# Performance work log

Measured on AMD Instinct MI355X. Metric: run time of the kernel, lower is better.

Reference implementation:

```python
import jax, jax.numpy as jnp
import numpy as np

B, T, C = 4, 1024, 768
H, HS = 12, 64           # num_heads, head_size
VD = 2 * HS              # value dim per head


def setup_inputs() -> dict:
    key = jax.random.key(0)
    ks = jax.random.split(key, 16)
    s = 0.02
    inp = {
        "x": jax.random.normal(ks[0], (B, T, C), jnp.float32),
        "Wq1": jax.random.normal(ks[1], (H, C, HS), jnp.float32) * s,
        "Wk1": jax.random.normal(ks[2], (H, C, HS), jnp.float32) * s,
        "Wq2": jax.random.normal(ks[3], (H, C, HS), jnp.float32) * s,
        "Wk2": jax.random.normal(ks[4], (H, C, HS), jnp.float32) * s,
        "Wv": jax.random.normal(ks[5], (H, C, VD), jnp.float32) * s,
        "lq1": jax.random.normal(ks[6], (H, HS), jnp.float32) * 0.1,
        "lk1": jax.random.normal(ks[7], (H, HS), jnp.float32) * 0.1,
        "lq2": jax.random.normal(ks[8], (H, HS), jnp.float32) * 0.1,
        "lk2": jax.random.normal(ks[9], (H, HS), jnp.float32) * 0.1,
        "gn_w": jnp.ones((H * VD,), jnp.float32),
        "gn_b": jnp.zeros((H * VD,), jnp.float32),
        "Wp": jax.random.normal(ks[10], (C, H * VD), jnp.float32) * s,
        "bp": jnp.zeros((C,), jnp.float32),
        "layer_idx": 3,
    }
    return inp


def _diff_attn(x, Wq1, Wk1, Wq2, Wk2, Wv, lq1, lk1, lq2, lk2,
               gn_w, gn_b, Wp, bp, layer_idx):
    Bc, Tc, _ = x.shape
    scale = 1.0 / jnp.sqrt(jnp.float32(HS))
    # per-head projections: [B,H,T,HS]
    q1 = jnp.einsum('btc,hcd->bhtd', x, Wq1)
    k1 = jnp.einsum('btc,hcd->bhtd', x, Wk1)
    q2 = jnp.einsum('btc,hcd->bhtd', x, Wq2)
    k2 = jnp.einsum('btc,hcd->bhtd', x, Wk2)
    v = jnp.einsum('btc,hce->bhte', x, Wv)           # [B,H,T,2HS]
    mask = jnp.tril(jnp.ones((Tc, Tc), bool))         # causal
    neg = jnp.float32(-jnp.inf)
    a1 = jnp.einsum('bhtd,bhsd->bhts', q1, k1) * scale
    a2 = jnp.einsum('bhtd,bhsd->bhts', q2, k2) * scale
    a1 = jax.nn.softmax(jnp.where(mask, a1, neg), axis=-1)
    a2 = jax.nn.softmax(jnp.where(mask, a2, neg), axis=-1)
    # dynamic lambda init, per get_lambda
    li = jnp.float32(layer_idx)
    dyn = 0.8 - 0.6 * jnp.exp(-0.3 * (li - 1.0))
    lam = jnp.mean(jnp.exp(lq1 * lk1) - jnp.exp(lq2 * lk2) + dyn, axis=-1)  # [H]
    diff = a1 - lam[None, :, None, None] * a2
    out = jnp.einsum('bhts,bhse->bhte', diff, v)      # [B,H,T,2HS]
    out = out.transpose(0, 2, 1, 3).reshape(Bc, Tc, H * VD)
    # GroupLayerNorm == full layernorm over last dim (unbiased=False var)
    mu = out.mean(-1, keepdims=True)
    var = jnp.mean((out - mu) ** 2, axis=-1, keepdims=True)
    out = (out - mu) / jnp.sqrt(var + 1e-5) * gn_w + gn_b
    out = out * 0.2  # (1 - lambda_init_buffer=0.8), buffer never updated
    return out @ Wp.T + bp


def reference(x, Wq1, Wk1, Wq2, Wk2, Wv, lq1, lk1, lq2, lk2,
              gn_w, gn_b, Wp, bp, layer_idx):
    return _diff_attn(x, Wq1, Wk1, Wq2, Wk2, Wv, lq1, lk1, lq2, lk2,
                      gn_w, gn_b, Wp, bp, layer_idx)
```

## Files before the change

### kernel.cpp

```cpp
#include <hip/hip_runtime.h>
#include <hip/hip_bf16.h>

#define Bc   4
#define Tc   1024
#define Cc   768
#define Hc   12
#define HSc  64
#define VDc  128
#define NQKV 4608
#define YLD  3072
#define NROWS 4096
#define HVD  1536

#define Q1OFF 0
#define K1OFF 768
#define Q2OFF 1536
#define K2OFF 2304

typedef __bf16 bf16x8 __attribute__((ext_vector_type(8)));
typedef float f32x4 __attribute__((ext_vector_type(4)));

#define PW_S 36
#define EXP2SCALE 0.18033688011112042f

static __device__ __forceinline__ float bf2f(unsigned short s) {
    return __uint_as_float(((unsigned int)s) << 16);
}
static __device__ __forceinline__ unsigned short f2bf(float f) {
    unsigned int u = __float_as_uint(f);
    unsigned int r = (u + 0x7FFFu + ((u >> 16) & 1u)) >> 16;
    return (unsigned short)r;
}
static __device__ __forceinline__ unsigned int pack2bf(float lo, float hi) {
    unsigned int a = (__float_as_uint(lo) + 0x8000u) >> 16;
    unsigned int b = (__float_as_uint(hi) + 0x8000u) & 0xFFFF0000u;
    return a | b;
}

static __device__ __forceinline__ void load16_lds(const void* g, void* l) {
    __builtin_amdgcn_global_load_lds(
        (const __attribute__((address_space(1))) void*)g,
        (__attribute__((address_space(3))) void*)l, 16, 0, 0);
}

__global__ __launch_bounds__(256) void cast_bf16(
    const float* __restrict__ src, unsigned short* __restrict__ dst)
{
    int i = blockIdx.x * 256 + threadIdx.x;
    float4 v = *(const float4*)(src + (size_t)i * 4);
    ushort4 u;
    u.x = f2bf(v.x); u.y = f2bf(v.y); u.z = f2bf(v.z); u.w = f2bf(v.w);
    *(ushort4*)(dst + (size_t)i * 4) = u;
}

__global__ __launch_bounds__(256) void trans_w(
    const float* __restrict__ Wq1, const float* __restrict__ Wk1,
    const float* __restrict__ Wq2, const float* __restrict__ Wk2,
    const float* __restrict__ Wv, unsigned short* __restrict__ WcatT)
{
    __shared__ float tile[64][65];
    int tid = threadIdx.x;
    int t = blockIdx.x;
    int kt = t % 12, nt = t / 12;
    int k0 = kt * 64, n0 = nt * 64;
    const float* src;
    int stride;
    if (n0 < 3072) {
        int which = n0 / 768, m = n0 - which * 768, h = m >> 6;
        const float* W = (which == 0) ? Wq1 : (which == 1) ? Wk1 : (which == 2) ? Wq2 : Wk2;
        src = W + ((size_t)h * 768 + k0) * 64;
        stride = 64;
    } else {
        int rel = n0 - 3072, h = rel >> 7, e0 = rel & 127;
        src = Wv + ((size_t)h * 768 + k0) * 128 + e0;
        stride = 128;
    }
    for (int i = tid; i < 4096; i += 256) {
        int kl = i >> 6, dl = i & 63;
        tile[dl][kl] = src[(size_t)kl * stride + dl];
    }
    __syncthreads();
    for (int i = tid; i < 4096; i += 256) {
        int nl = i >> 6, kl = i & 63;
        WcatT[(size_t)(n0 + nl) * 768 + k0 + kl] = f2bf(tile[nl][kl]);
    }
}

__global__ __launch_bounds__(64) void lambda_kernel(
    const float* __restrict__ lq1, const float* __restrict__ lk1,
    const float* __restrict__ lq2, const float* __restrict__ lk2,
    const int* __restrict__ layer_idx, float* __restrict__ lam)
{
    int h = blockIdx.x, l = threadIdx.x;
    float li = (float)layer_idx[0];
    float dyn = 0.8f - 0.6f * expf(-0.3f * (li - 1.0f));
    int i = h * HSc + l;
    float v = expf(lq1[i] * lk1[i]) - expf(lq2[i] * lk2[i]) + dyn;
    #pragma unroll
    for (int off = 32; off; off >>= 1) v += __shfl_xor(v, off);
    if (l == 0) lam[h] = v * (1.0f / 64.0f);
}

template<int TN, int KD, int LDC, bool OUT_BIAS, bool SPLITV>
__global__ __launch_bounds__(256) void gemm_mfma(
    const unsigned short* __restrict__ A, const unsigned short* __restrict__ Bt,
    unsigned short* __restrict__ Cb, float* __restrict__ Cf,
    const float* __restrict__ bias, unsigned short* __restrict__ VtOut)
{
    constexpr int BN = TN * 32;
    constexpr int JB = TN / 2;
    __shared__ unsigned short As[128 * 32];
    __shared__ unsigned short Bs[BN * 32];
    int tid = threadIdx.x, lane = tid & 63, w = tid >> 6;
    int wm = w >> 1, wn = w & 1;
    int m0 = blockIdx.y * 128, n0 = blockIdx.x * BN;

    int lr = lane >> 2, lq = lane & 3;
    const unsigned short* gA[2];
    const unsigned short* gB[JB];
    #pragma unroll
    for (int j = 0; j < 2; ++j) {
        int row = w * 32 + j * 16 + lr;
        int qg = lq ^ ((row >> 1) & 3);
        gA[j] = A + (size_t)(m0 + row) * KD + qg * 8;
    }
    #pragma unroll
    for (int j = 0; j < JB; ++j) {
        int row = w * (JB * 16) + j * 16 + lr;
        int qg = lq ^ ((row >> 1) & 3);
        gB[j] = Bt + (size_t)(n0 + row) * KD + qg * 8;
    }

    int rr = lane & 15, qd = lane >> 4;
    const unsigned short* aAddr[4];
    const unsigned short* bAddr[TN];
    #pragma unroll
    for (int i = 0; i < 4; ++i) {
        int row = wm * 64 + i * 16 + rr;
        int qs = qd ^ ((row >> 1) & 3);
        aAddr[i] = As + row * 32 + qs * 8;
    }
    #pragma unroll
    for (int t = 0; t < TN; ++t) {
        int row = wn * (TN * 16) + t * 16 + rr;
        int qs = qd ^ ((row >> 1) & 3);
        bAddr[t] = Bs + row * 32 + qs * 8;
    }

    f32x4 acc[4][TN];
    #pragma unroll
    for (int i = 0; i < 4; ++i)
        #pragma unroll
        for (int t = 0; t < TN; ++t) acc[i][t] = {0.f, 0.f, 0.f, 0.f};

    for (int k = 0; k < KD / 32; ++k) {
        __syncthreads();
        load16_lds(gA[0], As + (w * 2 + 0) * 512);
        load16_lds(gA[1], As + (w * 2 + 1) * 512);
        #pragma unroll
        for (int j = 0; j < JB; ++j)
            load16_lds(gB[j], Bs + (w * JB + j) * 512);
        gA[0] += 32; gA[1] += 32;
        #pragma unroll
        for (int j = 0; j < JB; ++j) gB[j] += 32;
        __syncthreads();

        bf16x8 af[4], bfr[TN];
        #pragma unroll
        for (int i = 0; i < 4; ++i) af[i] = *(const bf16x8*)aAddr[i];
        #pragma unroll
        for (int t = 0; t < TN; ++t) bfr[t] = *(const bf16x8*)bAddr[t];
        #pragma unroll
        for (int i = 0; i < 4; ++i)
            #pragma unroll
            for (int t = 0; t < TN; ++t)
                acc[i][t] = __builtin_amdgcn_mfma_f32_16x16x32_bf16(af[i], bfr[t], acc[i][t], 0, 0, 0);
    }

    #pragma unroll
    for (int t = 0; t < TN; ++t) {
        int col = n0 + wn * (TN * 16) + t * 16 + rr;
        if (SPLITV && col >= 3072) {
            int rel = col - 3072, hh = rel >> 7, e = rel & 127;
            #pragma unroll
            for (int i = 0; i < 4; ++i) {
                int row0 = m0 + wm * 64 + i * 16 + qd * 4;
                int b = row0 >> 10, tt = row0 & 1023;
                ushort4 pk;
                pk.x = f2bf(acc[i][t][0]); pk.y = f2bf(acc[i][t][1]);
                pk.z = f2bf(acc[i][t][2]); pk.w = f2bf(acc[i][t][3]);
                *(ushort4*)&VtOut[(size_t)((b * Hc + hh) * 128 + e) * 1024 + tt] = pk;
            }
        } else {
            float bv = OUT_BIAS ? bias[col] : 0.f;
            #pragma unroll
            for (int i = 0; i < 4; ++i) {
                #pragma unroll
                for (int r = 0; r < 4; ++r) {
                    int row = m0 + wm * 64 + i * 16 + qd * 4 + r;
                    if (OUT_BIAS)
                        Cf[(size_t)row * LDC + col] = acc[i][t][r] + bv;
                    else
                        Cb[(size_t)row * LDC + col] = f2bf(acc[i][t][r]);
                }
            }
        }
    }
}

__global__ __launch_bounds__(128, 2) void diff_attn_mfma(
    const unsigned short* __restrict__ Y, const unsigned short* __restrict__ Vt,
    const float* __restrict__ lam_buf, unsigned short* __restrict__ attn)
{
    __shared__ unsigned int PL32[2][16 * PW_S];
    int bh = blockIdx.x;
    int b = bh / Hc, h = bh - b * Hc;
    int QT = 31 - (int)blockIdx.y;
    int tid = threadIdx.x, lane = tid & 63, wv = tid >> 6;
    int cl = lane & 15, qd = lane >> 4;
    float lamv = lam_buf[h];
    size_t rowbase = (size_t)(b * Tc) * YLD;
    const int hq = h * HSc;
    unsigned int* Pw = PL32[wv];
    const unsigned short* VtB = Vt + ((size_t)bh << 17);
    const f32x4 zero4 = {0.f, 0.f, 0.f, 0.f};

    bf16x8 ka[2][4], kb[2][4], va[8], vb2[8];

    auto loadK = [&](int kt, bf16x8 kf[2][4]) {
        #pragma unroll
        for (int c = 0; c < 2; ++c) {
            size_t koff = rowbase + (size_t)(kt * 32 + c * 16 + cl) * YLD;
            kf[c][0] = *(const bf16x8*)(Y + koff + K1OFF + hq + qd * 8);
            kf[c][1] = *(const bf16x8*)(Y + koff + K1OFF + hq + 32 + qd * 8);
            kf[c][2] = *(const bf16x8*)(Y + koff + K2OFF + hq + qd * 8);
            kf[c][3] = *(const bf16x8*)(Y + koff + K2OFF + hq + 32 + qd * 8);
        }
    };
    auto loadV = [&](int kt, bf16x8 vf[8]) {
        #pragma unroll
        for (int ec = 0; ec < 8; ++ec)
            vf[ec] = *(const bf16x8*)(VtB + (((ec * 16 + cl) << 10) + kt * 32 + qd * 8));
    };

    int qrow = QT * 32 + wv * 16;

    size_t qoff = rowbase + (size_t)(qrow + cl) * YLD;
    bf16x8 q1a = *(const bf16x8*)(Y + qoff + Q1OFF + hq + qd * 8);
    bf16x8 q1b = *(const bf16x8*)(Y + qoff + Q1OFF + hq + 32 + qd * 8);
    bf16x8 q2a = *(const bf16x8*)(Y + qoff + Q2OFF + hq + qd * 8);
    bf16x8 q2b = *(const bf16x8*)(Y + qoff + Q2OFF + hq + 32 + qd * 8);

    f32x4 O1[8], O2[8];
    #pragma unroll
    for (int ec = 0; ec < 8; ++ec) { O1[ec] = zero4; O2[ec] = zero4; }
    float l1[4] = {0.f, 0.f, 0.f, 0.f}, l2[4] = {0.f, 0.f, 0.f, 0.f};

    auto tile = [&](int kt, bf16x8 kf[2][4], bf16x8 vf[8], bool diag) {
        f32x4 S1[2], S2[2];
        #pragma unroll
        for (int c = 0; c < 2; ++c) { S1[c] = zero4; S2[c] = zero4; }
        #pragma unroll
        for (int c = 0; c < 2; ++c) {
            S1[c] = __builtin_amdgcn_mfma_f32_16x16x32_bf16(q1a, kf[c][0], S1[c], 0, 0, 0);
            S1[c] = __builtin_amdgcn_mfma_f32_16x16x32_bf16(q1b, kf[c][1], S1[c], 0, 0, 0);
            S2[c] = __builtin_amdgcn_mfma_f32_16x16x32_bf16(q2a, kf[c][2], S2[c], 0, 0, 0);
            S2[c] = __builtin_amdgcn_mfma_f32_16x16x32_bf16(q2b, kf[c][3], S2[c], 0, 0, 0);
        }
        if (diag) {
            #pragma unroll
            for (int c = 0; c < 2; ++c) {
                int key_local = c * 16 + cl;
                #pragma unroll
                for (int r = 0; r < 4; ++r) {
                    int row_local = wv * 16 + qd * 4 + r;
                    if (key_local > row_local) { S1[c][r] = -1e30f; S2[c][r] = -1e30f; }
                }
            }
        }
        #pragma unroll
        for (int r = 0; r < 4; ++r) {
            float p10 = exp2f(S1[0][r] * EXP2SCALE);
            float p11 = exp2f(S1[1][r] * EXP2SCALE);
            float p20 = exp2f(S2[0][r] * EXP2SCALE);
            float p21 = exp2f(S2[1][r] * EXP2SCALE);
            l1[r] += p10 + p11;
            l2[r] += p20 + p21;
            int row = (qd << 2) + r;
            Pw[row * PW_S + cl]      = pack2bf(p10, p20);
            Pw[row * PW_S + cl + 16] = pack2bf(p11, p21);
        }
        const unsigned int* rp = Pw + cl * PW_S + qd * 8;
        uint4 L0 = *(const uint4*)(rp);
        uint4 L1 = *(const uint4*)(rp + 4);
        uint4 u1, u2;
        u1.x = __builtin_amdgcn_perm(L0.y, L0.x, 0x05040100u);
        u1.y = __builtin_amdgcn_perm(L0.w, L0.z, 0x05040100u);
        u1.z = __builtin_amdgcn_perm(L1.y, L1.x, 0x05040100u);
        u1.w = __builtin_amdgcn_perm(L1.w, L1.z, 0x05040100u);
        u2.x = __builtin_amdgcn_perm(L0.y, L0.x, 0x07060302u);
        u2.y = __builtin_amdgcn_perm(L0.w, L0.z, 0x07060302u);
        u2.z = __builtin_amdgcn_perm(L1.y, L1.x, 0x07060302u);
        u2.w = __builtin_amdgcn_perm(L1.w, L1.z, 0x07060302u);
        bf16x8 pa1 = __builtin_bit_cast(bf16x8, u1);
        bf16x8 pa2 = __builtin_bit_cast(bf16x8, u2);
        #pragma unroll
        for (int ec = 0; ec < 8; ++ec) {
            O1[ec] = __builtin_amdgcn_mfma_f32_16x16x32_bf16(pa1, vf[ec], O1[ec], 0, 0, 0);
            O2[ec] = __builtin_amdgcn_mfma_f32_16x16x32_bf16(pa2, vf[ec], O2[ec], 0, 0, 0);
        }
    };

    loadK(0, ka); loadV(0, va);
    for (int kt = 0; kt <= QT; kt += 2) {
        if (kt + 1 <= QT) { loadK(kt + 1, kb); loadV(kt + 1, vb2); }
        tile(kt, ka, va, kt == QT);
        if (kt + 1 <= QT) {
            if (kt + 2 <= QT) { loadK(kt + 2, ka); loadV(kt + 2, va); }
            tile(kt + 1, kb, vb2, kt + 1 == QT);
        }
    }

    float w1[4], w2[4];
    #pragma unroll
    for (int r = 0; r < 4; ++r) {
        float a = l1[r], c = l2[r];
        a += __shfl_xor(a, 1); a += __shfl_xor(a, 2);
        a += __shfl_xor(a, 4); a += __shfl_xor(a, 8);
        c += __shfl_xor(c, 1); c += __shfl_xor(c, 2);
        c += __shfl_xor(c, 4); c += __shfl_xor(c, 8);
        w1[r] = 1.0f / a;
        w2[r] = lamv / c;
    }
    #pragma unroll
    for (int ec = 0; ec < 8; ++ec) {
        #pragma unroll
        for (int r = 0; r < 4; ++r) {
            size_t row = (size_t)(b * Tc + qrow + qd * 4 + r);
            attn[row * HVD + h * VDc + ec * 16 + cl] =
                f2bf(O1[ec][r] * w1[r] - O2[ec][r] * w2[r]);
        }
    }
}

__global__ __launch_bounds__(128) void ln_inplace(
    unsigned short* __restrict__ attn,
    const float* __restrict__ gnw, const float* __restrict__ gnb)
{
    int row = blockIdx.x, tid = threadIdx.x;
    unsigned short* p = attn + (size_t)row * HVD;
    float v[12];
    float s = 0.f, sq = 0.f;
    #pragma unroll
    for (int j = 0; j < 3; ++j) {
        int g = tid + j * 128;
        ushort4 u = *(const ushort4*)(p + g * 4);
        float x0 = bf2f(u.x), x1 = bf2f(u.y), x2 = bf2f(u.z), x3 = bf2f(u.w);
        v[j * 4 + 0] = x0; v[j * 4 + 1] = x1; v[j * 4 + 2] = x2; v[j * 4 + 3] = x3;
        s += x0 + x1 + x2 + x3;
        sq = fmaf(x0, x0, sq); sq = fmaf(x1, x1, sq);
        sq = fmaf(x2, x2, sq); sq = fmaf(x3, x3, sq);
    }
    #pragma unroll
    for (int off = 32; off; off >>= 1) { s += __shfl_xor(s, off); sq += __shfl_xor(sq, off); }
    __shared__ float ss[2], sqs[2];
    if ((tid & 63) == 0) { ss[tid >> 6] = s; sqs[tid >> 6] = sq; }
    __syncthreads();
    float S = ss[0] + ss[1], Q = sqs[0] + sqs[1];
    float mu = S * (1.0f / HVD);
    float rstd = rsqrtf(Q * (1.0f / HVD) - mu * mu + 1e-5f);
    #pragma unroll
    for (int j = 0; j < 3; ++j) {
        int g = tid + j * 128;
        float4 gw = *(const float4*)(gnw + g * 4);
        float4 gb = *(const float4*)(gnb + g * 4);
        ushort4 o;
        o.x = f2bf(((v[j * 4 + 0] - mu) * rstd * gw.x + gb.x) * 0.2f);
        o.y = f2bf(((v[j * 4 + 1] - mu) * rstd * gw.y + gb.y) * 0.2f);
        o.z = f2bf(((v[j * 4 + 2] - mu) * rstd * gw.z + gb.z) * 0.2f);
        o.w = f2bf(((v[j * 4 + 3] - mu) * rstd * gw.w + gb.w) * 0.2f);
        *(ushort4*)(p + g * 4) = o;
    }
}

extern "C" void kernel_launch(void* const* d_in, const int* in_sizes, int n_in,
                              void* d_out, int out_size, void* d_ws, size_t ws_size,
                              hipStream_t stream)
{
    const float* x   = (const float*)d_in[0];
    const float* Wq1 = (const float*)d_in[1];
    const float* Wk1 = (const float*)d_in[2];
    const float* Wq2 = (const float*)d_in[3];
    const float* Wk2 = (const float*)d_in[4];
    const float* Wv  = (const float*)d_in[5];
    const float* lq1 = (const float*)d_in[6];
    const float* lk1 = (const float*)d_in[7];
    const float* lq2 = (const float*)d_in[8];
    const float* lk2 = (const float*)d_in[9];
    const float* gnw = (const float*)d_in[10];
    const float* gnb = (const float*)d_in[11];
    const float* Wp  = (const float*)d_in[12];
    const float* bp  = (const float*)d_in[13];
    const int*   lidx = (const int*)d_in[14];
    float* out = (float*)d_out;

    char* w = (char*)d_ws;
    unsigned short* WcatT = (unsigned short*)(w);
    unsigned short* Xb    = (unsigned short*)(w + 7077888);
    unsigned short* Y     = (unsigned short*)(w + 13369344);
    unsigned short* VtW   = (unsigned short*)(w + 38535168);
    unsigned short* attn  = (unsigned short*)(w + 51118080);
    unsigned short* Wpb   = (unsigned short*)(w + 63700992);
    float* lam            = (float*)(w + 66060288);

    cast_bf16<<<dim3(NROWS * Cc / 1024), 256, 0, stream>>>(x, Xb);
    cast_bf16<<<dim3(Cc * HVD / 1024), 256, 0, stream>>>(Wp, Wpb);
    trans_w<<<dim3(72 * 12), 256, 0, stream>>>(Wq1, Wk1, Wq2, Wk2, Wv, WcatT);
    lambda_kernel<<<dim3(Hc), 64, 0, stream>>>(lq1, lk1, lq2, lk2, lidx, lam);
    gemm_mfma<4, 768, YLD, false, true><<<dim3(NQKV / 128, NROWS / 128), 256, 0, stream>>>(
        Xb, WcatT, Y, nullptr, nullptr, VtW);
    diff_attn_mfma<<<dim3(Bc * Hc, 32), 128, 0, stream>>>(Y, VtW, lam, attn);
    ln_inplace<<<dim3(NROWS), 128, 0, stream>>>(attn, gnw, gnb);
    gemm_mfma<2, HVD, Cc, true, false><<<dim3(Cc / 64, NROWS / 128), 256, 0, stream>>>(
        attn, Wpb, nullptr, out, bp, nullptr);
}
```

Before: 292.3 us.

## Split attention key range across two wave pairs and reduce via LDS

The attention kernel now launches 256 threads per block: each pair of waves processes half of the key tiles for the same 32 query rows, a split-K over the causal key range. Partial O1/O2 accumulators and row sums from the second half are exchanged through shared memory and added by the first half, which then normalizes and writes the output. This doubles the waves available per block to hide latency and shortens the per-wave serial loop for long rows, at the cost of extra LDS traffic, three block barriers and higher shared memory use per block. No max-subtraction is used, so the partial sums combine without any rescaling.

```diff
diff --git a/kernel.cpp b/kernel.cpp
--- a/kernel.cpp
+++ b/kernel.cpp
@@ -208,15 +208,20 @@
     }
 }
 
-__global__ __launch_bounds__(128, 2) void diff_attn_mfma(
+__global__ __launch_bounds__(256, 4) void diff_attn_mfma(
     const unsigned short* __restrict__ Y, const unsigned short* __restrict__ Vt,
     const float* __restrict__ lam_buf, unsigned short* __restrict__ attn)
 {
-    __shared__ unsigned int PL32[2][16 * PW_S];
+    __shared__ __align__(16) unsigned int PL32[4][16 * PW_S];
+    __shared__ __align__(16) float Oex[2][128][20];
+    __shared__ float lex[2][16][2];
+
     int bh = blockIdx.x;
     int b = bh / Hc, h = bh - b * Hc;
     int QT = 31 - (int)blockIdx.y;
     int tid = threadIdx.x, lane = tid & 63, wv = tid >> 6;
+    int rg = wv & 1;
+    int sh = wv >> 1;
     int cl = lane & 15, qd = lane >> 4;
     float lamv = lam_buf[h];
     size_t rowbase = (size_t)(b * Tc) * YLD;
@@ -243,7 +248,7 @@
             vf[ec] = *(const bf16x8*)(VtB + (((ec * 16 + cl) << 10) + kt * 32 + qd * 8));
     };
 
-    int qrow = QT * 32 + wv * 16;
+    int qrow = QT * 32 + rg * 16;
 
     size_t qoff = rowbase + (size_t)(qrow + cl) * YLD;
     bf16x8 q1a = *(const bf16x8*)(Y + qoff + Q1OFF + hq + qd * 8);
@@ -273,7 +278,7 @@
                 int key_local = c * 16 + cl;
                 #pragma unroll
                 for (int r = 0; r < 4; ++r) {
-                    int row_local = wv * 16 + qd * 4 + r;
+                    int row_local = rg * 16 + qd * 4 + r;
                     if (key_local > row_local) { S1[c][r] = -1e30f; S2[c][r] = -1e30f; }
                 }
             }
@@ -311,17 +316,22 @@
         }
     };
 
-    loadK(0, ka); loadV(0, va);
-    for (int kt = 0; kt <= QT; kt += 2) {
-        if (kt + 1 <= QT) { loadK(kt + 1, kb); loadV(kt + 1, vb2); }
+    int n = QT + 1;
+    int nh = (n + 1) >> 1;
+    int lo = sh ? nh : 0;
+    int hi = sh ? n : nh;
+
+    if (lo < hi) { loadK(lo, ka); loadV(lo, va); }
+    for (int kt = lo; kt < hi; kt += 2) {
+        if (kt + 1 < hi) { loadK(kt + 1, kb); loadV(kt + 1, vb2); }
         tile(kt, ka, va, kt == QT);
-        if (kt + 1 <= QT) {
-            if (kt + 2 <= QT) { loadK(kt + 2, ka); loadV(kt + 2, va); }
+        if (kt + 1 < hi) {
+            if (kt + 2 < hi) { loadK(kt + 2, ka); loadV(kt + 2, va); }
             tile(kt + 1, kb, vb2, kt + 1 == QT);
         }
     }
 
-    float w1[4], w2[4];
+    float la1[4], la2[4];
     #pragma unroll
     for (int r = 0; r < 4; ++r) {
         float a = l1[r], c = l2[r];
@@ -329,16 +339,58 @@
         a += __shfl_xor(a, 4); a += __shfl_xor(a, 8);
         c += __shfl_xor(c, 1); c += __shfl_xor(c, 2);
         c += __shfl_xor(c, 4); c += __shfl_xor(c, 8);
-        w1[r] = 1.0f / a;
-        w2[r] = lamv / c;
-    }
-    #pragma unroll
-    for (int ec = 0; ec < 8; ++ec) {
+        la1[r] = a; la2[r] = c;
+    }
+
+    if (sh == 1) {
+        #pragma unroll
+        for (int ec = 0; ec < 8; ++ec)
+            *(f32x4*)&Oex[rg][ec * 16 + cl][qd * 4] = O1[ec];
+        if (cl == 0) {
+            #pragma unroll
+            for (int r = 0; r < 4; ++r) {
+                lex[rg][qd * 4 + r][0] = la1[r];
+                lex[rg][qd * 4 + r][1] = la2[r];
+            }
+        }
+    }
+    __syncthreads();
+    if (sh == 0) {
+        #pragma unroll
+        for (int ec = 0; ec < 8; ++ec)
+            O1[ec] += *(const f32x4*)&Oex[rg][ec * 16 + cl][qd * 4];
         #pragma unroll
         for (int r = 0; r < 4; ++r) {
-            size_t row = (size_t)(b * Tc + qrow + qd * 4 + r);
-            attn[row * HVD + h * VDc + ec * 16 + cl] =
-                f2bf(O1[ec][r] * w1[r] - O2[ec][r] * w2[r]);
+            la1[r] += lex[rg][qd * 4 + r][0];
+            la2[r] += lex[rg][qd * 4 + r][1];
+        }
+    }
+    __syncthreads();
+    if (sh == 1) {
+        #pragma unroll
+        for (int ec = 0; ec < 8; ++ec)
+            *(f32x4*)&Oex[rg][ec * 16 + cl][qd * 4] = O2[ec];
+    }
+    __syncthreads();
+    if (sh == 0) {
+        #pragma unroll
+        for (int ec = 0; ec < 8; ++ec)
+            O2[ec] += *(const f32x4*)&Oex[rg][ec * 16 + cl][qd * 4];
+
+        float w1[4], w2[4];
+        #pragma unroll
+        for (int r = 0; r < 4; ++r) {
+            w1[r] = 1.0f / la1[r];
+            w2[r] = lamv / la2[r];
+        }
+        #pragma unroll
+        for (int ec = 0; ec < 8; ++ec) {
+            #pragma unroll
+            for (int r = 0; r < 4; ++r) {
+                size_t row = (size_t)(b * Tc + qrow + qd * 4 + r);
+                attn[row * HVD + h * VDc + ec * 16 + cl] =
+                    f2bf(O1[ec][r] * w1[r] - O2[ec][r] * w2[r]);
+            }
         }
     }
 }
@@ -419,7 +471,7 @@
     lambda_kernel<<<dim3(Hc), 64, 0, stream>>>(lq1, lk1, lq2, lk2, lidx, lam);
     gemm_mfma<4, 768, YLD, false, true><<<dim3(NQKV / 128, NROWS / 128), 256, 0, stream>>>(
         Xb, WcatT, Y, nullptr, nullptr, VtW);
-    diff_attn_mfma<<<dim3(Bc * Hc, 32), 128, 0, stream>>>(Y, VtW, lam, attn);
+    diff_attn_mfma<<<dim3(Bc * Hc, 32), 256, 0, stream>>>(Y, VtW, lam, attn);
     ln_inplace<<<dim3(NROWS), 128, 0, stream>>>(attn, gnw, gnb);
     gemm_mfma<2, HVD, Cc, true, false><<<dim3(Cc / 64, NROWS / 128), 256, 0, stream>>>(
         attn, Wpb, nullptr, out, bp, nullptr);
```

Result: slower. 482.6 us (+65.1%).

## Stage K/V tiles through swizzled shared memory shared by four-wave query blocks

Applied to the files above, without the earlier changes.

The attention kernel now processes 64 query rows per block with four waves. K and V tiles are staged cooperatively into double-buffered, XOR-swizzled LDS via direct global-to-LDS loads, and all waves read their fragments from there. Before, each wave loaded its own K/V fragments from global memory into registers. The aim is to cut redundant global K/V traffic and raise reuse, at the cost of a block-wide barrier per key tile and idle waves on the diagonal tail.

```diff
diff --git a/kernel.cpp b/kernel.cpp
--- a/kernel.cpp
+++ b/kernel.cpp
@@ -208,14 +208,16 @@
     }
 }
 
-__global__ __launch_bounds__(128, 2) void diff_attn_mfma(
+__global__ __launch_bounds__(256) void diff_attn_mfma(
     const unsigned short* __restrict__ Y, const unsigned short* __restrict__ Vt,
     const float* __restrict__ lam_buf, unsigned short* __restrict__ attn)
 {
-    __shared__ unsigned int PL32[2][16 * PW_S];
+    __shared__ __align__(16) unsigned short KV[2][8192];
+    __shared__ __align__(16) unsigned int PL32[4][16 * PW_S];
+
     int bh = blockIdx.x;
     int b = bh / Hc, h = bh - b * Hc;
-    int QT = 31 - (int)blockIdx.y;
+    int g = 15 - (int)blockIdx.y;
     int tid = threadIdx.x, lane = tid & 63, wv = tid >> 6;
     int cl = lane & 15, qd = lane >> 4;
     float lamv = lam_buf[h];
@@ -225,25 +227,57 @@
     const unsigned short* VtB = Vt + ((size_t)bh << 17);
     const f32x4 zero4 = {0.f, 0.f, 0.f, 0.f};
 
-    bf16x8 ka[2][4], kb[2][4], va[8], vb2[8];
-
-    auto loadK = [&](int kt, bf16x8 kf[2][4]) {
-        #pragma unroll
-        for (int c = 0; c < 2; ++c) {
-            size_t koff = rowbase + (size_t)(kt * 32 + c * 16 + cl) * YLD;
-            kf[c][0] = *(const bf16x8*)(Y + koff + K1OFF + hq + qd * 8);
-            kf[c][1] = *(const bf16x8*)(Y + koff + K1OFF + hq + 32 + qd * 8);
-            kf[c][2] = *(const bf16x8*)(Y + koff + K2OFF + hq + qd * 8);
-            kf[c][3] = *(const bf16x8*)(Y + koff + K2OFF + hq + 32 + qd * 8);
+    int ksrow = lane >> 3;
+    int ksch  = (lane & 7) ^ ksrow;
+    int offk[4];
+    {
+        int mat = wv & 1;
+        int moff = mat ? K2OFF : K1OFF;
+        #pragma unroll
+        for (int r8 = 0; r8 < 4; ++r8)
+            offk[r8] = (r8 * 8 + ksrow) * YLD + moff + hq + ksch * 8;
+    }
+    int vsel = lane >> 2;
+    int vsch = (lane & 3) ^ (vsel & 3);
+    int offv[4];
+    {
+        int sv0 = (wv & 1) * 4;
+        #pragma unroll
+        for (int i = 0; i < 4; ++i)
+            offv[i] = ((sv0 + i) * 16 + vsel) * 1024 + vsch * 8;
+    }
+
+    auto stage = [&](int kt, int cur) {
+        char* base = (char*)KV[cur] + wv * 4096;
+        if (wv < 2) {
+            const unsigned short* g0 = Y + rowbase + (size_t)(kt * 32) * YLD;
+            #pragma unroll
+            for (int r8 = 0; r8 < 4; ++r8)
+                load16_lds(g0 + offk[r8], base + r8 * 1024);
+        } else {
+            const unsigned short* g0 = VtB + kt * 32;
+            #pragma unroll
+            for (int i = 0; i < 4; ++i)
+                load16_lds(g0 + offv[i], base + i * 1024);
         }
     };
-    auto loadV = [&](int kt, bf16x8 vf[8]) {
-        #pragma unroll
-        for (int ec = 0; ec < 8; ++ec)
-            vf[ec] = *(const bf16x8*)(VtB + (((ec * 16 + cl) << 10) + kt * 32 + qd * 8));
-    };
-
-    int qrow = QT * 32 + wv * 16;
+
+    int kfo[2][4], vfo[8];
+    #pragma unroll
+    for (int c = 0; c < 2; ++c) {
+        int row = c * 16 + cl;
+        #pragma unroll
+        for (int j = 0; j < 4; ++j)
+            kfo[c][j] = (j >> 1) * 4096 + row * 128 +
+                        ((((j & 1) * 4 + qd) ^ (row & 7)) << 4);
+    }
+    #pragma unroll
+    for (int ec = 0; ec < 8; ++ec) {
+        int e = ec * 16 + cl;
+        vfo[ec] = 8192 + e * 64 + ((qd ^ (e & 3)) << 4);
+    }
+
+    int qrow = g * 64 + wv * 16;
 
     size_t qoff = rowbase + (size_t)(qrow + cl) * YLD;
     bf16x8 q1a = *(const bf16x8*)(Y + qoff + Q1OFF + hq + qd * 8);
@@ -256,7 +290,15 @@
     for (int ec = 0; ec < 8; ++ec) { O1[ec] = zero4; O2[ec] = zero4; }
     float l1[4] = {0.f, 0.f, 0.f, 0.f}, l2[4] = {0.f, 0.f, 0.f, 0.f};
 
-    auto tile = [&](int kt, bf16x8 kf[2][4], bf16x8 vf[8], bool diag) {
+    auto tile = [&](int cur, int kt, bool diag) {
+        const char* kb = (const char*)KV[cur];
+        bf16x8 kf[2][4];
+        #pragma unroll
+        for (int c = 0; c < 2; ++c)
+            #pragma unroll
+            for (int j = 0; j < 4; ++j)
+                kf[c][j] = *(const bf16x8*)(kb + kfo[c][j]);
+
         f32x4 S1[2], S2[2];
         #pragma unroll
         for (int c = 0; c < 2; ++c) { S1[c] = zero4; S2[c] = zero4; }
@@ -270,14 +312,18 @@
         if (diag) {
             #pragma unroll
             for (int c = 0; c < 2; ++c) {
-                int key_local = c * 16 + cl;
+                int kq = kt * 32 + c * 16 + cl - qrow - qd * 4;
                 #pragma unroll
                 for (int r = 0; r < 4; ++r) {
-                    int row_local = wv * 16 + qd * 4 + r;
-                    if (key_local > row_local) { S1[c][r] = -1e30f; S2[c][r] = -1e30f; }
+                    if (kq > r) { S1[c][r] = -1e30f; S2[c][r] = -1e30f; }
                 }
             }
         }
+        bf16x8 vf[8];
+        #pragma unroll
+        for (int ec = 0; ec < 8; ++ec)
+            vf[ec] = *(const bf16x8*)(kb + vfo[ec]);
+
         #pragma unroll
         for (int r = 0; r < 4; ++r) {
             float p10 = exp2f(S1[0][r] * EXP2SCALE);
@@ -311,14 +357,19 @@
         }
     };
 
-    loadK(0, ka); loadV(0, va);
-    for (int kt = 0; kt <= QT; kt += 2) {
-        if (kt + 1 <= QT) { loadK(kt + 1, kb); loadV(kt + 1, vb2); }
-        tile(kt, ka, va, kt == QT);
-        if (kt + 1 <= QT) {
-            if (kt + 2 <= QT) { loadK(kt + 2, ka); loadV(kt + 2, va); }
-            tile(kt + 1, kb, vb2, kt + 1 == QT);
-        }
+    int NT = 2 * g + 2;
+    int ktmax = 2 * g + (wv >> 1);
+
+    stage(0, 0);
+    __syncthreads();
+    for (int kt = 0; kt < NT; ++kt) {
+        int cur = kt & 1;
+        if (kt + 1 < NT) stage(kt + 1, cur ^ 1);
+        if (kt <= ktmax) {
+            bool diag = (kt * 32 + 31 > qrow);
+            tile(cur, kt, diag);
+        }
+        __syncthreads();
     }
 
     float w1[4], w2[4];
@@ -419,7 +470,7 @@
     lambda_kernel<<<dim3(Hc), 64, 0, stream>>>(lq1, lk1, lq2, lk2, lidx, lam);
     gemm_mfma<4, 768, YLD, false, true><<<dim3(NQKV / 128, NROWS / 128), 256, 0, stream>>>(
         Xb, WcatT, Y, nullptr, nullptr, VtW);
-    diff_attn_mfma<<<dim3(Bc * Hc, 32), 128, 0, stream>>>(Y, VtW, lam, attn);
+    diff_attn_mfma<<<dim3(Bc * Hc, 16), 256, 0, stream>>>(Y, VtW, lam, attn);
     ln_inplace<<<dim3(NROWS), 128, 0, stream>>>(attn, gnw, gnb);
     gemm_mfma<2, HVD, Cc, true, false><<<dim3(Cc / 64, NROWS / 128), 256, 0, stream>>>(
         attn, Wpb, nullptr, out, bp, nullptr);
```

New measurement: 284.2 us. 1.03x faster.
